# Kernel optimization log

Measured on AMD Instinct MI355X. Metric: run time of the kernel, lower is better.

The kernel has to match this reference:

```python
import jax, jax.numpy as jnp
import numpy as np

N = 8192
F_IN = 128
F_OUT = 128
NEG_SLOPE = 0.2


def setup_inputs() -> dict:
    key = jax.random.key(0)
    k_h, k_adj, k_W, k_a = jax.random.split(key, 4)
    h = jax.random.normal(k_h, (N, F_IN), dtype=jnp.float32)
    # binary adjacency mask as float (the module multiplies scores by adj)
    adj = (jax.random.uniform(k_adj, (N, N)) < 0.05).astype(jnp.float32)
    # nn.Linear(in, out, bias=False): weight shape [out, in]
    W = jax.random.normal(k_W, (F_OUT, F_IN), dtype=jnp.float32) / np.sqrt(F_IN)
    # nn.Linear(2*out, 1, bias=False): weight shape [1, 2*out]
    a = jax.random.normal(k_a, (1, 2 * F_OUT), dtype=jnp.float32) / np.sqrt(2 * F_OUT)
    return {"h": h, "adj": adj, "W": W, "a": a}


def reference(h, adj, W, a):
    # Wh: [N, F_out]
    Wh = h @ W.T
    f = Wh.shape[-1]
    # a([Wh_i ; Wh_j]) factored: e[i, j] = leaky_relu(Wh[i]@a1 + Wh[j]@a2)
    a1 = a[0, :f]  # [F_out]
    a2 = a[0, f:]  # [F_out]
    s_i = Wh @ a1  # [N]
    s_j = Wh @ a2  # [N]
    e = jax.nn.leaky_relu(s_i[:, None] + s_j[None, :], NEG_SLOPE)  # [N, N]
    # faithful to original: softmax over dim=1 of e * adj (multiplicative mask)
    attention = jax.nn.softmax(e * adj, axis=1)  # [N, N]
    return attention @ Wh  # [N, F_out]
```

## Files before the change

### kernel.cpp

```cpp
#include <hip/hip_runtime.h>

#define N_NODES 8192
#define FDIM 128
#define NEG_SLOPE 0.2f

typedef short short8 __attribute__((ext_vector_type(8)));
typedef float floatx16 __attribute__((ext_vector_type(16)));
typedef unsigned long long u64;

static __device__ inline unsigned fkey(float x) {
  unsigned b = __float_as_uint(x);
  return (b & 0x80000000u) ? ~b : (b | 0x80000000u);
}
static __device__ inline float fkey_dec(unsigned kk) {
  unsigned bb = (kk & 0x80000000u) ? (kk ^ 0x80000000u) : ~kk;
  return __uint_as_float(bb);
}
static __device__ inline unsigned short bf16_rn(float x) {
  unsigned u = __float_as_uint(x);
  u += 0x7fffu + ((u >> 16) & 1u);
  return (unsigned short)(u >> 16);
}

__global__ __launch_bounds__(256) void wh_fused_kernel(
    const float* __restrict__ h, const float* __restrict__ W,
    const float* __restrict__ a, float* __restrict__ s1g,
    float* __restrict__ Bj, float* __restrict__ Dj, float* __restrict__ S,
    unsigned* __restrict__ s2max_key, unsigned short* __restrict__ WHf) {
  __shared__ float Wt[FDIM * 129];
  __shared__ float rows[32 * 132];
  const int t = threadIdx.x;
  const int base = blockIdx.x * 32;
  for (int it = 0; it < 64; ++it) {
    int idx = t + 256 * it;
    int o = idx >> 7, k = idx & 127;
    Wt[k * 129 + o] = W[idx];
  }
  for (int it = 0; it < 16; ++it) {
    int idx = t + 256 * it;
    int r = idx >> 7, col = idx & 127;
    rows[r * 132 + col] = h[(size_t)base * FDIM + idx];
  }
  __syncthreads();
  const int c4 = (t & 31) * 4;
  const int g = t >> 5;
  float acc[4][4];
#pragma unroll
  for (int rr = 0; rr < 4; ++rr)
#pragma unroll
    for (int cc = 0; cc < 4; ++cc) acc[rr][cc] = 0.f;
  for (int k = 0; k < FDIM; ++k) {
    float4 wv = *(const float4*)&Wt[k * 129 + c4];
    float rv[4];
#pragma unroll
    for (int rr = 0; rr < 4; ++rr) rv[rr] = rows[(4 * g + rr) * 132 + k];
#pragma unroll
    for (int rr = 0; rr < 4; ++rr) {
      acc[rr][0] += rv[rr] * wv.x;
      acc[rr][1] += rv[rr] * wv.y;
      acc[rr][2] += rv[rr] * wv.z;
      acc[rr][3] += rv[rr] * wv.w;
    }
  }
  {
    float4 a1c = *(const float4*)&a[c4];
    float4 a2c = *(const float4*)&a[FDIM + c4];
    float p1[4], p2[4];
#pragma unroll
    for (int rr = 0; rr < 4; ++rr) {
      p1[rr] = acc[rr][0] * a1c.x + acc[rr][1] * a1c.y +
               acc[rr][2] * a1c.z + acc[rr][3] * a1c.w;
      p2[rr] = acc[rr][0] * a2c.x + acc[rr][1] * a2c.y +
               acc[rr][2] * a2c.z + acc[rr][3] * a2c.w;
    }
#pragma unroll
    for (int rr = 0; rr < 4; ++rr)
      for (int off = 16; off; off >>= 1) {
        p1[rr] += __shfl_down(p1[rr], off, 32);
        p2[rr] += __shfl_down(p2[rr], off, 32);
      }
    if ((t & 31) == 0) {
      unsigned kmax = 0;
#pragma unroll
      for (int rr = 0; rr < 4; ++rr) {
        int r = base + 4 * g + rr;
        s1g[r] = p1[rr];
        Bj[r] = __expf(p2[rr]);
        Dj[r] = __expf(NEG_SLOPE * p2[rr]);
        unsigned kk = fkey(p2[rr]);
        kmax = kk > kmax ? kk : kmax;
      }
      atomicMax(s2max_key, kmax);
    }
  }
  __syncthreads();
  unsigned short* hbuf = (unsigned short*)Wt;
#pragma unroll
  for (int rr = 0; rr < 4; ++rr)
#pragma unroll
    for (int cc = 0; cc < 4; ++cc) {
      int lr = 4 * g + rr;
      int n = c4 + cc;
      int idx = (((lr >> 4) * 4 + (n >> 5)) * 64 + ((lr >> 3) & 1) * 32 +
                 (n & 31)) * 8 + (lr & 7);
      hbuf[idx] = bf16_rn(acc[rr][cc]);
    }
  float4 cs = make_float4(acc[0][0] + acc[1][0] + acc[2][0] + acc[3][0],
                          acc[0][1] + acc[1][1] + acc[2][1] + acc[3][1],
                          acc[0][2] + acc[1][2] + acc[2][2] + acc[3][2],
                          acc[0][3] + acc[1][3] + acc[2][3] + acc[3][3]);
  *(float4*)&rows[g * FDIM + c4] = cs;
  __syncthreads();
  {
    const unsigned* hsrc = (const unsigned*)hbuf;
    unsigned* hdst = (unsigned*)(WHf + (size_t)base * FDIM);
    for (int q = t; q < 2048; q += 256) hdst[q] = hsrc[q];
  }
  if (t < FDIM) {
    float s = 0.f;
#pragma unroll
    for (int gg = 0; gg < 8; ++gg) s += rows[gg * FDIM + t];
    atomicAdd(&S[t], s);
  }
}

__global__ __launch_bounds__(256) void gat_mfma_kernel(
    const float* __restrict__ adj, const unsigned short* __restrict__ WHf,
    const float* __restrict__ s1g, const float* __restrict__ Bj,
    const float* __restrict__ Dj, const unsigned* __restrict__ s2max_key,
    float* __restrict__ num, float* __restrict__ l_ws) {
  __shared__ u64 bits[4][32][4];
  __shared__ float cred[32 * FDIM];
  const int t = threadIdx.x;
  const int lane = t & 63;
  const int wave = t >> 6;
  const int lq = lane & 31, hh = lane >> 5;
  const int rowgrp = blockIdx.x >> 2;
  const int ksplit = blockIdx.x & 3;
  const int grow = rowgrp * 32;
  const int kw0 = ksplit * 2048 + wave * 512;

  for (int q = t; q < 32 * FDIM; q += 256) cred[q] = 0.f;
  __syncthreads();

  const float s2m = fkey_dec(*s2max_key);
  const float s1r = s1g[grow + lq];
  float pm = s1r + s2m;
  pm = pm > 0.f ? pm : NEG_SLOPE * pm;
  const float mr = fmaxf(pm, 0.f);
  const float emr = __expf(-mr);
  const float Ar = __expf(s1r - mr);
  const float Cr = __expf(NEG_SLOPE * s1r - mr);
  const float Tr = __expf(-s1r);

  const short8* BW = (const short8*)WHf;
  floatx16 acc[4];
#pragma unroll
  for (int nt = 0; nt < 4; ++nt)
#pragma unroll
    for (int i = 0; i < 16; ++i) acc[nt][i] = 0.f;
  float lv = 0.f;
  u64* mybits = &bits[wave][0][0];

  for (int s = 0; s < 2; ++s) {
    const int c0 = kw0 + s * 256;
    const float4* ap = (const float4*)(adj + (size_t)grow * N_NODES + c0);
#pragma unroll 2
    for (int rb = 0; rb < 32; rb += 8) {
      float4 va[8];
#pragma unroll
      for (int r = 0; r < 8; ++r)
        va[r] = ap[(size_t)(rb + r) * (N_NODES / 4) + lane];
#pragma unroll
      for (int r = 0; r < 8; ++r) {
        u64 b0 = __ballot(va[r].x != 0.f);
        u64 b1 = __ballot(va[r].y != 0.f);
        u64 b2 = __ballot(va[r].z != 0.f);
        u64 b3 = __ballot(va[r].w != 0.f);
        if (lane == 0) {
          u64* d = &mybits[(rb + r) * 4];
          d[0] = b0; d[1] = b1; d[2] = b2; d[3] = b3;
        }
      }
    }
    ulonglong2 q0 = *(const ulonglong2*)&mybits[lq * 4];
    ulonglong2 q1 = *(const ulonglong2*)&mybits[lq * 4 + 2];
    const u64 ws0 = q0.x, ws1 = q0.y, ws2 = q1.x, ws3 = q1.y;
#pragma unroll 2
    for (int it = 0; it < 16; ++it) {
      const int kg = c0 + it * 16;
      const int j8 = kg + hh * 8;
      float4 b0 = *(const float4*)(Bj + j8);
      float4 b1 = *(const float4*)(Bj + j8 + 4);
      float4 d0 = *(const float4*)(Dj + j8);
      float4 d1 = *(const float4*)(Dj + j8 + 4);
      size_t fb = (size_t)(kg >> 4) * 256 + lane;
      short8 x0 = BW[fb];
      short8 x1 = BW[fb + 64];
      short8 x2 = BW[fb + 128];
      short8 x3 = BW[fb + 192];
      float bvv[8] = {b0.x, b0.y, b0.z, b0.w, b1.x, b1.y, b1.z, b1.w};
      float dvv[8] = {d0.x, d0.y, d0.z, d0.w, d1.x, d1.y, d1.z, d1.w};
      const u64 wsel[4] = {ws0, ws1, ws2, ws3};
      const int bsh = it * 4 + hh * 2;
      float vv[8];
#pragma unroll
      for (int e = 0; e < 8; ++e) {
        unsigned bit = (unsigned)(wsel[e & 3] >> (bsh + (e >> 2))) & 1u;
        bool cp = bvv[e] > Tr;
        float q = (cp ? Ar : Cr) * (cp ? bvv[e] : dvv[e]);
        float v = bit ? (q - emr) : 0.f;
        vv[e] = v;
        lv += v;
      }
      union { uint4 u; short8 s8; } pk;
      pk.u.x = (unsigned)bf16_rn(vv[0]) | ((unsigned)bf16_rn(vv[1]) << 16);
      pk.u.y = (unsigned)bf16_rn(vv[2]) | ((unsigned)bf16_rn(vv[3]) << 16);
      pk.u.z = (unsigned)bf16_rn(vv[4]) | ((unsigned)bf16_rn(vv[5]) << 16);
      pk.u.w = (unsigned)bf16_rn(vv[6]) | ((unsigned)bf16_rn(vv[7]) << 16);
      short8 af = pk.s8;
      acc[0] = __builtin_amdgcn_mfma_f32_32x32x16_bf16(af, x0, acc[0], 0, 0, 0);
      acc[1] = __builtin_amdgcn_mfma_f32_32x32x16_bf16(af, x1, acc[1], 0, 0, 0);
      acc[2] = __builtin_amdgcn_mfma_f32_32x32x16_bf16(af, x2, acc[2], 0, 0, 0);
      acc[3] = __builtin_amdgcn_mfma_f32_32x32x16_bf16(af, x3, acc[3], 0, 0, 0);
    }
  }
  float lvt = lv + __shfl_xor(lv, 32);
  if (lane < 32) atomicAdd(&l_ws[grow + lq], lvt);
#pragma unroll
  for (int reg = 0; reg < 16; ++reg) {
    const int r = (reg & 3) + 8 * (reg >> 2) + 4 * hh;
#pragma unroll
    for (int nt = 0; nt < 4; ++nt)
      atomicAdd(&cred[r * FDIM + nt * 32 + lq], acc[nt][reg]);
  }
  __syncthreads();
  for (int q = t; q < 32 * FDIM; q += 256)
    atomicAdd(&num[(size_t)(grow + (q >> 7)) * FDIM + (q & 127)], cred[q]);
}

__global__ __launch_bounds__(256) void norm_kernel(
    const float* __restrict__ num, const float* __restrict__ l_ws,
    const float* __restrict__ s1g, const unsigned* __restrict__ s2max_key,
    const float* __restrict__ S, float* __restrict__ out) {
  const int idx = blockIdx.x * 256 + threadIdx.x;
  const int row = idx >> 5;
  const float s2m = fkey_dec(*s2max_key);
  float s1r = s1g[row];
  float pm = s1r + s2m;
  pm = pm > 0.f ? pm : NEG_SLOPE * pm;
  float mr = fmaxf(pm, 0.f);
  float em = __expf(-mr);
  float l = (float)N_NODES * em + l_ws[row];
  float inv = 1.f / l;
  float4 nv = ((const float4*)num)[idx];
  float4 Sv = ((const float4*)S)[idx & 31];
  ((float4*)out)[idx] = make_float4((nv.x + em * Sv.x) * inv,
                                    (nv.y + em * Sv.y) * inv,
                                    (nv.z + em * Sv.z) * inv,
                                    (nv.w + em * Sv.w) * inv);
}

extern "C" void kernel_launch(void* const* d_in, const int* in_sizes, int n_in,
                              void* d_out, int out_size, void* d_ws, size_t ws_size,
                              hipStream_t stream) {
  const float* h   = (const float*)d_in[0];
  const float* adj = (const float*)d_in[1];
  const float* W   = (const float*)d_in[2];
  const float* a   = (const float*)d_in[3];
  float* out = (float*)d_out;
  float* num = (float*)d_ws;
  float* l_ws = num + (size_t)N_NODES * FDIM;
  float* S = l_ws + N_NODES;
  unsigned* key = (unsigned*)(S + FDIM);
  float* s1 = (float*)(key + 4);
  float* Bj = s1 + N_NODES;
  float* Dj = Bj + N_NODES;
  unsigned short* WHf = (unsigned short*)(Dj + N_NODES);

  hipMemsetAsync(num, 0,
                 ((size_t)N_NODES * FDIM + N_NODES + FDIM + 4) * sizeof(float),
                 stream);
  hipLaunchKernelGGL(wh_fused_kernel, dim3(N_NODES / 32), dim3(256), 0, stream,
                     h, W, a, s1, Bj, Dj, S, key, WHf);
  hipLaunchKernelGGL(gat_mfma_kernel, dim3(1024), dim3(256), 0, stream,
                     adj, WHf, s1, Bj, Dj, key, num, l_ws);
  hipLaunchKernelGGL(norm_kernel, dim3(N_NODES * FDIM / 4 / 256), dim3(256), 0,
                     stream, num, l_ws, s1, key, S, out);
}
```

Before: 490.2 us.

## Pack adjacency into bitmask in a separate pass and accumulate directly into output

New measurement: 507.7 us. 1.04x slower.

```diff
diff --git a/kernel.cpp b/kernel.cpp
--- a/kernel.cpp
+++ b/kernel.cpp
@@ -124,12 +124,31 @@
   }
 }
 
+__global__ __launch_bounds__(256) void pack_kernel(
+    const float4* __restrict__ adj4, u64* __restrict__ bits) {
+  const int t0 = blockIdx.x * 256 + threadIdx.x;
+  const int lane = threadIdx.x & 63;
+#pragma unroll 4
+  for (int it = 0; it < 32; ++it) {
+    const int idx = t0 + it * (2048 * 256);
+    float4 v = adj4[idx];
+    u64 b0 = __ballot(v.x != 0.f);
+    u64 b1 = __ballot(v.y != 0.f);
+    u64 b2 = __ballot(v.z != 0.f);
+    u64 b3 = __ballot(v.w != 0.f);
+    const int ub = (idx - lane) >> 4;
+    if (lane < 4) {
+      u64 bs = lane == 0 ? b0 : lane == 1 ? b1 : lane == 2 ? b2 : b3;
+      bits[ub + lane] = bs;
+    }
+  }
+}
+
 __global__ __launch_bounds__(256) void gat_mfma_kernel(
-    const float* __restrict__ adj, const unsigned short* __restrict__ WHf,
+    const u64* __restrict__ bits, const unsigned short* __restrict__ WHf,
     const float* __restrict__ s1g, const float* __restrict__ Bj,
     const float* __restrict__ Dj, const unsigned* __restrict__ s2max_key,
     float* __restrict__ num, float* __restrict__ l_ws) {
-  __shared__ u64 bits[4][32][4];
   __shared__ float cred[32 * FDIM];
   const int t = threadIdx.x;
   const int lane = t & 63;
@@ -154,37 +173,19 @@
   const float Tr = __expf(-s1r);
 
   const short8* BW = (const short8*)WHf;
+  const u64* myrow = bits + (size_t)(grow + lq) * (N_NODES / 64);
   floatx16 acc[4];
 #pragma unroll
   for (int nt = 0; nt < 4; ++nt)
 #pragma unroll
     for (int i = 0; i < 16; ++i) acc[nt][i] = 0.f;
   float lv = 0.f;
-  u64* mybits = &bits[wave][0][0];
 
   for (int s = 0; s < 2; ++s) {
     const int c0 = kw0 + s * 256;
-    const float4* ap = (const float4*)(adj + (size_t)grow * N_NODES + c0);
-#pragma unroll 2
-    for (int rb = 0; rb < 32; rb += 8) {
-      float4 va[8];
-#pragma unroll
-      for (int r = 0; r < 8; ++r)
-        va[r] = ap[(size_t)(rb + r) * (N_NODES / 4) + lane];
-#pragma unroll
-      for (int r = 0; r < 8; ++r) {
-        u64 b0 = __ballot(va[r].x != 0.f);
-        u64 b1 = __ballot(va[r].y != 0.f);
-        u64 b2 = __ballot(va[r].z != 0.f);
-        u64 b3 = __ballot(va[r].w != 0.f);
-        if (lane == 0) {
-          u64* d = &mybits[(rb + r) * 4];
-          d[0] = b0; d[1] = b1; d[2] = b2; d[3] = b3;
-        }
-      }
-    }
-    ulonglong2 q0 = *(const ulonglong2*)&mybits[lq * 4];
-    ulonglong2 q1 = *(const ulonglong2*)&mybits[lq * 4 + 2];
+    const u64* bp = myrow + (c0 >> 6);
+    ulonglong2 q0 = *(const ulonglong2*)bp;
+    ulonglong2 q1 = *(const ulonglong2*)(bp + 2);
     const u64 ws0 = q0.x, ws1 = q0.y, ws2 = q1.x, ws3 = q1.y;
 #pragma unroll 2
     for (int it = 0; it < 16; ++it) {
@@ -240,9 +241,9 @@
 }
 
 __global__ __launch_bounds__(256) void norm_kernel(
-    const float* __restrict__ num, const float* __restrict__ l_ws,
+    float* __restrict__ numout, const float* __restrict__ l_ws,
     const float* __restrict__ s1g, const unsigned* __restrict__ s2max_key,
-    const float* __restrict__ S, float* __restrict__ out) {
+    const float* __restrict__ S) {
   const int idx = blockIdx.x * 256 + threadIdx.x;
   const int row = idx >> 5;
   const float s2m = fkey_dec(*s2max_key);
@@ -253,12 +254,12 @@
   float em = __expf(-mr);
   float l = (float)N_NODES * em + l_ws[row];
   float inv = 1.f / l;
-  float4 nv = ((const float4*)num)[idx];
+  float4 nv = ((float4*)numout)[idx];
   float4 Sv = ((const float4*)S)[idx & 31];
-  ((float4*)out)[idx] = make_float4((nv.x + em * Sv.x) * inv,
-                                    (nv.y + em * Sv.y) * inv,
-                                    (nv.z + em * Sv.z) * inv,
-                                    (nv.w + em * Sv.w) * inv);
+  ((float4*)numout)[idx] = make_float4((nv.x + em * Sv.x) * inv,
+                                       (nv.y + em * Sv.y) * inv,
+                                       (nv.z + em * Sv.z) * inv,
+                                       (nv.w + em * Sv.w) * inv);
 }
 
 extern "C" void kernel_launch(void* const* d_in, const int* in_sizes, int n_in,
@@ -269,22 +270,23 @@
   const float* W   = (const float*)d_in[2];
   const float* a   = (const float*)d_in[3];
   float* out = (float*)d_out;
-  float* num = (float*)d_ws;
-  float* l_ws = num + (size_t)N_NODES * FDIM;
+  u64* bits = (u64*)d_ws;
+  unsigned short* WHf = (unsigned short*)(bits + (size_t)(N_NODES / 64) * N_NODES);
+  float* l_ws = (float*)(WHf + (size_t)N_NODES * FDIM);
   float* S = l_ws + N_NODES;
   unsigned* key = (unsigned*)(S + FDIM);
   float* s1 = (float*)(key + 4);
   float* Bj = s1 + N_NODES;
   float* Dj = Bj + N_NODES;
-  unsigned short* WHf = (unsigned short*)(Dj + N_NODES);
-
-  hipMemsetAsync(num, 0,
-                 ((size_t)N_NODES * FDIM + N_NODES + FDIM + 4) * sizeof(float),
-                 stream);
+
+  hipMemsetAsync(out, 0, (size_t)N_NODES * FDIM * sizeof(float), stream);
+  hipMemsetAsync(l_ws, 0, (N_NODES + FDIM + 4) * sizeof(float), stream);
+  hipLaunchKernelGGL(pack_kernel, dim3(2048), dim3(256), 0, stream,
+                     (const float4*)adj, bits);
   hipLaunchKernelGGL(wh_fused_kernel, dim3(N_NODES / 32), dim3(256), 0, stream,
                      h, W, a, s1, Bj, Dj, S, key, WHf);
   hipLaunchKernelGGL(gat_mfma_kernel, dim3(1024), dim3(256), 0, stream,
-                     adj, WHf, s1, Bj, Dj, key, num, l_ws);
+                     bits, WHf, s1, Bj, Dj, key, out, l_ws);
   hipLaunchKernelGGL(norm_kernel, dim3(N_NODES * FDIM / 4 / 256), dim3(256), 0,
-                     stream, num, l_ws, s1, key, S, out);
-}
+                     stream, out, l_ws, s1, key, S);
+}
```
